# Performance work log

Measured on AMD Instinct MI355X. Metric: run time of the kernel, lower is better.

The kernel has to match this reference:

```python
import jax, jax.numpy as jnp
import numpy as np

# ---- constants (match init_kwargs) ----
H = 16            # bit depth of location codes
TP = 8            # number of parallel location dims
N = 1 << H        # location magnitude bound
N_K = 2
N_C = 2 * H * N_K + 1   # 65 candidate locations per token
T = 512           # T_train
N_TTNBR = 64
K_VOCAB = 128
S = N_TTNBR + K_VOCAB   # 192
D = 256           # dim_eu
TEMP = 0.05


def cos_similarity(c1, c2):
    """CritiGraph frexp-based cosine: sign product * (1 - bitlength(|a|^|b| + 1)/h)."""
    sg = (2 * (c1 >= 0).astype(jnp.int32) - 1) * (2 * (c2 >= 0).astype(jnp.int32) - 1)
    x = jnp.abs(c1) ^ jnp.abs(c2)
    _, e = jnp.frexp((x + 1).astype(jnp.float32))  # exponent == bit_length(x+1)
    return sg.astype(jnp.float32) * (1.0 - e.astype(jnp.float32) / H)


def setup_inputs() -> dict:
    key = jax.random.key(0)
    ks = jax.random.split(key, 8)
    loc = lambda k, shape: jax.random.randint(k, shape, 1 - N, N, dtype=jnp.int32)
    return {
        "cur_tar": jax.random.randint(ks[0], (T,), 0, K_VOCAB, dtype=jnp.int32),
        "cnc_loc": loc(ks[1], (T, N_C, TP)),
        "sta_loc": loc(ks[2], (T, TP)),
        "ttn_loc": loc(ks[3], (T, N_TTNBR, TP)),
        "voc_loc": loc(ks[4], (T, K_VOCAB, TP)),
        "sta_emb": 0.1 * jax.random.normal(ks[5], (T, D), dtype=jnp.float32),
        "ttn_emb": 0.1 * jax.random.normal(ks[6], (T, N_TTNBR, D), dtype=jnp.float32),
        "voc_emb": 0.1 * jax.random.normal(ks[7], (T, K_VOCAB, D), dtype=jnp.float32),
    }


def reference(cur_tar, cnc_loc, sta_loc, ttn_loc, voc_loc, sta_emb, ttn_emb, voc_emb):
    # positives = dynamic neighbors ++ sampled vocab
    pos_loc = jnp.concatenate([ttn_loc, voc_loc], axis=1)      # (T, S, TP) int32
    pos_emb = jnp.concatenate([ttn_emb, voc_emb], axis=1)      # (T, S, D)

    # Euclidean-space logits
    eu_val = 20.0 * TEMP * jnp.einsum('td,tsd->ts', sta_emb, pos_emb)  # (T, S)

    # CT-space similarities
    cos_sp = cos_similarity(sta_loc[:, None, :], pos_loc)      # (T, S, TP)
    cos_sum = cos_sp.sum(axis=-1)                              # (T, S)
    # candidate location swapped into each track d (ct_val_triton math)
    cos_cp = cos_similarity(cnc_loc[:, None, :, :], pos_loc[:, :, None, :])  # (T, S, N_C, TP)
    ct_val = (cos_sum[:, :, None, None] - cos_sp[:, :, None, :] + cos_cp) / TP \
             * (20.0 * TEMP)                                   # (T, S, N_C, TP)

    # KL(eu || ct) over the dynamic neighbors
    logits_ct_dyn = ct_val[:, :N_TTNBR]                        # (T, Nn, N_C, TP)
    logits_eu_dyn = eu_val[:, :N_TTNBR]                        # (T, Nn)
    p_eu = jax.nn.softmax(logits_eu_dyn, axis=1)
    lp_eu = jax.nn.log_softmax(logits_eu_dyn, axis=1)
    lp_ct = jax.nn.log_softmax(logits_ct_dyn, axis=1)
    loss_dyn_dyn = (p_eu[:, :, None, None] * (lp_eu[:, :, None, None] - lp_ct)).sum(axis=1)  # (T, N_C, TP)

    # cross-entropy over the sampled vocab
    logits_ct_sta = ct_val[:, N_TTNBR:] / TEMP                 # (T, K, N_C, TP)
    logits_flat = logits_ct_sta.reshape(T, K_VOCAB, N_C * TP)
    log_probs = jax.nn.log_softmax(logits_flat, axis=1)        # (T, K, N_C*TP)
    idx = jnp.broadcast_to(cur_tar[:, None, None].astype(jnp.int32), (T, 1, N_C * TP))
    target_lp = jnp.take_along_axis(log_probs, idx, axis=1)[:, 0, :]  # (T, N_C*TP)
    loss_dyn_sta = -target_lp.reshape(T, N_C, TP)              # (T, N_C, TP)

    return loss_dyn_dyn, loss_dyn_sta
```

## Files before the change

### kernel.cpp

```cpp
#include <hip/hip_runtime.h>


#define Tn   512
#define NC   65
#define TPd  8
#define NTn  64
#define KV   128
#define Sn   192
#define Dn   256
#define OUT1 (Tn * NC * TPd)
#define TABN 34
#define TABR (TABN * 32)

#define LOG2E 1.44269504088896340736f
#define LN2   0.69314718055994530942f
#define K1S (0.0625f * 2.5f * LOG2E)
#define K0S (-2.5f * LOG2E)

__device__ __forceinline__ float exp2_fast(float x) {
#if __has_builtin(__builtin_amdgcn_exp2f)
    return __builtin_amdgcn_exp2f(x);
#else
    return exp2f(x);
#endif
}
__device__ __forceinline__ int pack_loc(int v) {
    return (v < 0) ? (int)(0x80000000u | (unsigned)(-v)) : v;
}
__device__ __forceinline__ float asf(int v) { return __int_as_float(v); }

__device__ __forceinline__ float cos_raw(int y) {
    int   x = (y & 0x7fffffff) + 1;
    float c = fmaf((float)__clz(x), 0.0625f, -1.0f);
    return __int_as_float(__float_as_int(c) ^ (y & 0x80000000));
}
__device__ __forceinline__ int tab_idx(int y) {
    int x = (y & 0x7fffffff) + 1;
    int u = __clz(x) - 15;
    return u * 2 + (int)(((unsigned)y) >> 31);
}

__global__ __launch_bounds__(512, 4) void critigraph_kernel(
    const int*   __restrict__ cur_tar,
    const int*   __restrict__ cnc_loc,
    const int*   __restrict__ sta_loc,
    const int*   __restrict__ ttn_loc,
    const int*   __restrict__ voc_loc,
    const float* __restrict__ sta_emb,
    const float* __restrict__ ttn_emb,
    float*       __restrict__ out)
{
    __shared__ int4  s_dyn4[NTn * TPd];
    __shared__ int2  s_sta2[KV * TPd];
    __shared__ float s_tab[3 * TABR];
    __shared__ int   s_cnc[NC * TPd];
    __shared__ int   s_staloc[TPd];
    __shared__ float s_csum[Sn];
    __shared__ float s_eu[NTn];
    __shared__ float s_peu[NTn];
    __shared__ float s_dotbase[TPd];
    __shared__ float s_kl;

    const int t   = blockIdx.x;
    const int tid = threadIdx.x;

    if (tid < TPd) s_staloc[tid] = pack_loc(sta_loc[t * TPd + tid]);
    for (int i = tid; i < NC * TPd; i += 512)
        s_cnc[i] = pack_loc(cnc_loc[t * NC * TPd + i]);
    for (int i = tid; i < TABR; i += 512) {
        int   idx = i >> 5;
        int   clz = 15 + (idx >> 1);
        float mag = (float)clz * 0.0625f - 1.0f;
        float sgn = (idx & 1) ? -1.f : 1.f;
        float ccd = sgn * mag * (0.125f * LOG2E);
        float ccs = sgn * mag * (2.5f * LOG2E);
        s_tab[i]            = exp2_fast(ccd);
        s_tab[i + TABR]     = ccd;
        s_tab[i + 2 * TABR] = exp2_fast(ccs);
    }
    __syncthreads();

    const int mysta = s_staloc[tid & 7];
    float mysp[3];
    #pragma unroll
    for (int k = 0; k < 3; ++k) {
        int i = tid + 512 * k;
        int s = i >> 3;
        int v = (s < NTn) ? ttn_loc[t * NTn * TPd + i]
                          : voc_loc[t * KV * TPd + (i - NTn * TPd)];
        int packed = pack_loc(v);
        float c = cos_raw(packed ^ mysta);
        mysp[k] = c;
        if (s < NTn) s_dyn4[i].x = packed;
        else         s_sta2[i - NTn * TPd].x = packed;
        float v8 = c;
        v8 += __shfl_xor(v8, 1);
        v8 += __shfl_xor(v8, 2);
        v8 += __shfl_xor(v8, 4);
        if ((tid & 7) == 0) s_csum[s] = v8;
    }
    {
        const int r = tid >> 3, q = tid & 7;
        const float4* A = (const float4*)(sta_emb + (size_t)t * Dn);
        const float4* B = (const float4*)(ttn_emb + ((size_t)t * NTn + r) * Dn);
        float acc = 0.f;
        #pragma unroll
        for (int k = 0; k < 8; ++k) {
            float4 a = A[k * 8 + q];
            float4 b = B[k * 8 + q];
            acc += a.x * b.x + a.y * b.y + a.z * b.z + a.w * b.w;
        }
        acc += __shfl_xor(acc, 1);
        acc += __shfl_xor(acc, 2);
        acc += __shfl_xor(acc, 4);
        if (q == 0) s_eu[r] = acc;
    }
    __syncthreads();

    #pragma unroll
    for (int k = 0; k < 3; ++k) {
        int i = tid + 512 * k;
        int s = i >> 3;
        if (s < NTn) {
            float b2 = (s_csum[s] - mysp[k]) * (0.125f * LOG2E);
            s_dyn4[i].y = __float_as_int(exp2_fast(b2));
            s_dyn4[i].w = __float_as_int(b2);
        } else {
            float b2 = (s_csum[s] - mysp[k]) * (2.5f * LOG2E);
            s_sta2[i - NTn * TPd].y = __float_as_int(exp2_fast(b2));
        }
    }
    if (tid < 64) {
        float e  = s_eu[tid];
        float mx = e;
        #pragma unroll
        for (int m = 1; m < 64; m <<= 1) mx = fmaxf(mx, __shfl_xor(mx, m));
        float ex = __expf(e - mx);
        float z  = ex;
        #pragma unroll
        for (int m = 1; m < 64; m <<= 1) z += __shfl_xor(z, m);
        float pe = ex / z;
        s_peu[tid] = pe;
        float kls = pe * ((e - mx) - __logf(z));
        #pragma unroll
        for (int m = 1; m < 64; m <<= 1) kls += __shfl_xor(kls, m);
        if (tid == 0) s_kl = kls;
    }
    __syncthreads();

    s_dyn4[tid].z = __float_as_int(s_peu[tid >> 3]);
    if (tid < 64) {
        int g = tid & 7, j = tid >> 3;
        float a = 0.f;
        #pragma unroll
        for (int k = 0; k < 8; ++k) {
            int s = 8 * j + k;
            a = fmaf(s_peu[s], asf(s_dyn4[s * TPd + g].w), a);
        }
        #pragma unroll
        for (int m = 8; m < 64; m <<= 1) a += __shfl_xor(a, m);
        if (tid < TPd) s_dotbase[g] = a;
    }
    __syncthreads();

    const int   p    = tid & 7;
    const int   acnc = s_cnc[tid];
    const int   tar  = cur_tar[t];
    const float kl   = s_kl;
    const float dtb  = s_dotbase[p];
    const float* tb  = s_tab + (tid & 31);

    float sum = 0.f, dot = 0.f;
    #pragma unroll 16
    for (int s = 0; s < NTn; ++s) {
        int4  ab  = s_dyn4[s * TPd + p];
        int   j   = tab_idx(ab.x ^ acnc) * 32;
        float eD  = tb[j];
        float ccD = tb[j + TABR];
        sum = fmaf(asf(ab.y), eD, sum);
        dot = fmaf(asf(ab.z), ccD, dot);
    }
    float s2 = 0.f;
    #pragma unroll 16
    for (int v = 0; v < KV; ++v) {
        int2  ab = s_sta2[v * TPd + p];
        int   j  = tab_idx(ab.x ^ acnc) * 32;
        s2 = fmaf(asf(ab.y), tb[j + 2 * TABR], s2);
    }
    {
        int   ax  = s_sta2[tar * TPd + p].x;
        float sp  = cos_raw(ax ^ s_staloc[p]);
        float b2t = (s_csum[NTn + tar] - sp) * (2.5f * LOG2E);
        int   y   = ax ^ acnc;
        int   x   = (y & 0x7fffffff) + 1;
        float cct = fmaf((float)__clz(x), K1S, K0S);
        cct = __int_as_float(__float_as_int(cct) ^ (y & 0x80000000));
        float* od = out + (size_t)t * NC * TPd;
        float* os = out + OUT1 + (size_t)t * NC * TPd;
        od[tid] = kl + LN2 * (__log2f(sum) - (dtb + dot));
        os[tid] = LN2 * (__log2f(s2) - (b2t + cct));
    }

    {
        const int w    = tid >> 6;
        const int lane = tid & 63;
        const int acw  = s_cnc[512 + w];
        float sumd, dotd, sums;
        {
            int4  ab = s_dyn4[lane * TPd + w];
            int   j  = tab_idx(ab.x ^ acw) * 32;
            sumd = asf(ab.y) * tb[j];
            dotd = asf(ab.z) * tb[j + TABR];
        }
        {
            int2 ab0 = s_sta2[lane * TPd + w];
            int2 ab1 = s_sta2[(lane + 64) * TPd + w];
            int  j0  = tab_idx(ab0.x ^ acw) * 32;
            int  j1  = tab_idx(ab1.x ^ acw) * 32;
            sums = asf(ab0.y) * tb[j0 + 2 * TABR] + asf(ab1.y) * tb[j1 + 2 * TABR];
        }
        #pragma unroll
        for (int m = 1; m < 64; m <<= 1) {
            sumd += __shfl_xor(sumd, m);
            dotd += __shfl_xor(dotd, m);
            sums += __shfl_xor(sums, m);
        }
        if (lane == 0) {
            int   ax  = s_sta2[tar * TPd + w].x;
            float sp  = cos_raw(ax ^ s_staloc[w]);
            float b2t = (s_csum[NTn + tar] - sp) * (2.5f * LOG2E);
            int   y   = ax ^ acw;
            int   x   = (y & 0x7fffffff) + 1;
            float cct = fmaf((float)__clz(x), K1S, K0S);
            cct = __int_as_float(__float_as_int(cct) ^ (y & 0x80000000));
            out[(size_t)t * NC * TPd + 512 + w] =
                kl + LN2 * (__log2f(sumd) - (s_dotbase[w] + dotd));
            out[OUT1 + (size_t)t * NC * TPd + 512 + w] =
                LN2 * (__log2f(sums) - (b2t + cct));
        }
    }
}

extern "C" void kernel_launch(void* const* d_in, const int* in_sizes, int n_in,
                              void* d_out, int out_size, void* d_ws, size_t ws_size,
                              hipStream_t stream) {
    (void)in_sizes; (void)n_in; (void)d_ws; (void)ws_size; (void)out_size;
    const int*   cur_tar = (const int*)  d_in[0];
    const int*   cnc_loc = (const int*)  d_in[1];
    const int*   sta_loc = (const int*)  d_in[2];
    const int*   ttn_loc = (const int*)  d_in[3];
    const int*   voc_loc = (const int*)  d_in[4];
    const float* sta_emb = (const float*)d_in[5];
    const float* ttn_emb = (const float*)d_in[6];
    critigraph_kernel<<<Tn, 512, 0, stream>>>(cur_tar, cnc_loc, sta_loc, ttn_loc,
                                              voc_loc, sta_emb, ttn_emb, (float*)d_out);
}
```

Measured before the change: 143.5 us.

## Replace LDS exp lookup tables with inline clz math and packed bf16 operands

Drops the per-block shared-memory lookup tables and computes the cosine term and its exp2 inline from clz on a new shifted sign-magnitude packing. Shared data is laid out so two positives sit in one int4, and the dynamic-neighbour exp and softmax weights are packed as two rounded 16-bit halves in one word. This halves LDS traffic in the main loops and removes the table-building pass, at the cost of more ALU and transcendental work per element. The bf16 rounding of the exp and probability factors lowers precision, which may break accuracy tolerances.

```diff
diff --git a/kernel.cpp b/kernel.cpp
--- a/kernel.cpp
+++ b/kernel.cpp
@@ -9,13 +9,12 @@
 #define Sn   192
 #define Dn   256
 #define OUT1 (Tn * NC * TPd)
-#define TABN 34
-#define TABR (TABN * 32)
 
 #define LOG2E 1.44269504088896340736f
 #define LN2   0.69314718055994530942f
-#define K1S (0.0625f * 2.5f * LOG2E)
-#define K0S (-2.5f * LOG2E)
+#define ADYN (0.125f * LOG2E * 0.0625f)
+#define ASTA (2.5f  * LOG2E * 0.0625f)
+#define ARAW 0.0625f
 
 __device__ __forceinline__ float exp2_fast(float x) {
 #if __has_builtin(__builtin_amdgcn_exp2f)
@@ -24,20 +23,21 @@
     return exp2f(x);
 #endif
 }
-__device__ __forceinline__ int pack_loc(int v) {
-    return (v < 0) ? (int)(0x80000000u | (unsigned)(-v)) : v;
-}
 __device__ __forceinline__ float asf(int v) { return __int_as_float(v); }
-
-__device__ __forceinline__ float cos_raw(int y) {
-    int   x = (y & 0x7fffffff) + 1;
-    float c = fmaf((float)__clz(x), 0.0625f, -1.0f);
-    return __int_as_float(__float_as_int(c) ^ (y & 0x80000000));
-}
-__device__ __forceinline__ int tab_idx(int y) {
-    int x = (y & 0x7fffffff) + 1;
-    int u = __clz(x) - 15;
-    return u * 2 + (int)(((unsigned)y) >> 31);
+__device__ __forceinline__ int   asi(float v) { return __float_as_int(v); }
+
+__device__ __forceinline__ int pack15(int v) {
+    int a = (v < 0) ? -v : v;
+    return (a << 15) | (int)(((unsigned)v) >> 31);
+}
+__device__ __forceinline__ float cos15(int y, float A) {
+    int   x = y + 0x8000;
+    float c = fmaf((float)__clz(x), A, -A);
+    return asf(asi(c) ^ (y << 31));
+}
+
+__device__ __forceinline__ int eidx(int s, int p) {
+    return ((s >> 1) * TPd + p) * 2 + (s & 1);
 }
 
 __global__ __launch_bounds__(512, 4) void critigraph_kernel(
@@ -50,9 +50,9 @@
     const float* __restrict__ ttn_emb,
     float*       __restrict__ out)
 {
-    __shared__ int4  s_dyn4[NTn * TPd];
+    __shared__ int2  s_dyn2[NTn * TPd];
     __shared__ int2  s_sta2[KV * TPd];
-    __shared__ float s_tab[3 * TABR];
+    __shared__ float s_b2d[NTn * TPd];
     __shared__ int   s_cnc[NC * TPd];
     __shared__ int   s_staloc[TPd];
     __shared__ float s_csum[Sn];
@@ -63,21 +63,11 @@
 
     const int t   = blockIdx.x;
     const int tid = threadIdx.x;
-
-    if (tid < TPd) s_staloc[tid] = pack_loc(sta_loc[t * TPd + tid]);
+    const int tar = cur_tar[t];
+
+    if (tid < TPd) s_staloc[tid] = pack15(sta_loc[t * TPd + tid]);
     for (int i = tid; i < NC * TPd; i += 512)
-        s_cnc[i] = pack_loc(cnc_loc[t * NC * TPd + i]);
-    for (int i = tid; i < TABR; i += 512) {
-        int   idx = i >> 5;
-        int   clz = 15 + (idx >> 1);
-        float mag = (float)clz * 0.0625f - 1.0f;
-        float sgn = (idx & 1) ? -1.f : 1.f;
-        float ccd = sgn * mag * (0.125f * LOG2E);
-        float ccs = sgn * mag * (2.5f * LOG2E);
-        s_tab[i]            = exp2_fast(ccd);
-        s_tab[i + TABR]     = ccd;
-        s_tab[i + 2 * TABR] = exp2_fast(ccs);
-    }
+        s_cnc[i] = pack15(cnc_loc[t * NC * TPd + i]);
     __syncthreads();
 
     const int mysta = s_staloc[tid & 7];
@@ -86,18 +76,19 @@
     for (int k = 0; k < 3; ++k) {
         int i = tid + 512 * k;
         int s = i >> 3;
+        int p = i & 7;
         int v = (s < NTn) ? ttn_loc[t * NTn * TPd + i]
                           : voc_loc[t * KV * TPd + (i - NTn * TPd)];
-        int packed = pack_loc(v);
-        float c = cos_raw(packed ^ mysta);
+        int packed = pack15(v);
+        float c = cos15(packed ^ mysta, ARAW);
         mysp[k] = c;
-        if (s < NTn) s_dyn4[i].x = packed;
-        else         s_sta2[i - NTn * TPd].x = packed;
+        if (s < NTn) s_dyn2[eidx(s, p)].x = packed;
+        else         s_sta2[eidx(s - NTn, p)].x = packed;
         float v8 = c;
         v8 += __shfl_xor(v8, 1);
         v8 += __shfl_xor(v8, 2);
         v8 += __shfl_xor(v8, 4);
-        if ((tid & 7) == 0) s_csum[s] = v8;
+        if (p == 0) s_csum[s] = v8;
     }
     {
         const int r = tid >> 3, q = tid & 7;
@@ -121,13 +112,15 @@
     for (int k = 0; k < 3; ++k) {
         int i = tid + 512 * k;
         int s = i >> 3;
+        int p = i & 7;
         if (s < NTn) {
             float b2 = (s_csum[s] - mysp[k]) * (0.125f * LOG2E);
-            s_dyn4[i].y = __float_as_int(exp2_fast(b2));
-            s_dyn4[i].w = __float_as_int(b2);
+            int   e  = eidx(s, p);
+            s_dyn2[e].y = asi(exp2_fast(b2));
+            s_b2d[e]    = b2;
         } else {
             float b2 = (s_csum[s] - mysp[k]) * (2.5f * LOG2E);
-            s_sta2[i - NTn * TPd].y = __float_as_int(exp2_fast(b2));
+            s_sta2[eidx(s - NTn, p)].y = asi(exp2_fast(b2));
         }
     }
     if (tid < 64) {
@@ -148,14 +141,21 @@
     }
     __syncthreads();
 
-    s_dyn4[tid].z = __float_as_int(s_peu[tid >> 3]);
+    {
+        int i = tid;
+        int s = (((i >> 4) << 1) | (i & 1));
+        int Eb = s_dyn2[i].y;
+        int Pb = asi(s_peu[s]);
+        s_dyn2[i].y = (int)((((unsigned)Eb + 0x8000u) & 0xFFFF0000u) |
+                            (((unsigned)Pb + 0x8000u) >> 16));
+    }
     if (tid < 64) {
         int g = tid & 7, j = tid >> 3;
         float a = 0.f;
         #pragma unroll
         for (int k = 0; k < 8; ++k) {
             int s = 8 * j + k;
-            a = fmaf(s_peu[s], asf(s_dyn4[s * TPd + g].w), a);
+            a = fmaf(s_peu[s], s_b2d[eidx(s, g)], a);
         }
         #pragma unroll
         for (int m = 8; m < 64; m <<= 1) a += __shfl_xor(a, m);
@@ -165,36 +165,43 @@
 
     const int   p    = tid & 7;
     const int   acnc = s_cnc[tid];
-    const int   tar  = cur_tar[t];
     const float kl   = s_kl;
     const float dtb  = s_dotbase[p];
-    const float* tb  = s_tab + (tid & 31);
+    const int4* dyn4 = (const int4*)s_dyn2;
+    const int4* sta4 = (const int4*)s_sta2;
 
     float sum = 0.f, dot = 0.f;
-    #pragma unroll 16
-    for (int s = 0; s < NTn; ++s) {
-        int4  ab  = s_dyn4[s * TPd + p];
-        int   j   = tab_idx(ab.x ^ acnc) * 32;
-        float eD  = tb[j];
-        float ccD = tb[j + TABR];
-        sum = fmaf(asf(ab.y), eD, sum);
-        dot = fmaf(asf(ab.z), ccD, dot);
+    #pragma unroll 8
+    for (int j = 0; j < NTn / 2; ++j) {
+        int4 q = dyn4[j * TPd + p];
+        {
+            int   y  = q.x ^ acnc;
+            float cc = cos15(y, ADYN);
+            float E  = asf(q.y & (int)0xFFFF0000);
+            float pe = asf(q.y << 16);
+            sum = fmaf(E, exp2_fast(cc), sum);
+            dot = fmaf(pe, cc, dot);
+        }
+        {
+            int   y  = q.z ^ acnc;
+            float cc = cos15(y, ADYN);
+            float E  = asf(q.w & (int)0xFFFF0000);
+            float pe = asf(q.w << 16);
+            sum = fmaf(E, exp2_fast(cc), sum);
+            dot = fmaf(pe, cc, dot);
+        }
     }
     float s2 = 0.f;
-    #pragma unroll 16
-    for (int v = 0; v < KV; ++v) {
-        int2  ab = s_sta2[v * TPd + p];
-        int   j  = tab_idx(ab.x ^ acnc) * 32;
-        s2 = fmaf(asf(ab.y), tb[j + 2 * TABR], s2);
-    }
-    {
-        int   ax  = s_sta2[tar * TPd + p].x;
-        float sp  = cos_raw(ax ^ s_staloc[p]);
-        float b2t = (s_csum[NTn + tar] - sp) * (2.5f * LOG2E);
-        int   y   = ax ^ acnc;
-        int   x   = (y & 0x7fffffff) + 1;
-        float cct = fmaf((float)__clz(x), K1S, K0S);
-        cct = __int_as_float(__float_as_int(cct) ^ (y & 0x80000000));
+    #pragma unroll 8
+    for (int j = 0; j < KV / 2; ++j) {
+        int4 q = sta4[j * TPd + p];
+        s2 = fmaf(asf(q.y), exp2_fast(cos15(q.x ^ acnc, ASTA)), s2);
+        s2 = fmaf(asf(q.w), exp2_fast(cos15(q.z ^ acnc, ASTA)), s2);
+    }
+    {
+        int2  tq  = s_sta2[eidx(tar, p)];
+        float b2t = __log2f(asf(tq.y));
+        float cct = cos15(tq.x ^ acnc, ASTA);
         float* od = out + (size_t)t * NC * TPd;
         float* os = out + OUT1 + (size_t)t * NC * TPd;
         od[tid] = kl + LN2 * (__log2f(sum) - (dtb + dot));
@@ -207,17 +214,17 @@
         const int acw  = s_cnc[512 + w];
         float sumd, dotd, sums;
         {
-            int4  ab = s_dyn4[lane * TPd + w];
-            int   j  = tab_idx(ab.x ^ acw) * 32;
-            sumd = asf(ab.y) * tb[j];
-            dotd = asf(ab.z) * tb[j + TABR];
-        }
-        {
-            int2 ab0 = s_sta2[lane * TPd + w];
-            int2 ab1 = s_sta2[(lane + 64) * TPd + w];
-            int  j0  = tab_idx(ab0.x ^ acw) * 32;
-            int  j1  = tab_idx(ab1.x ^ acw) * 32;
-            sums = asf(ab0.y) * tb[j0 + 2 * TABR] + asf(ab1.y) * tb[j1 + 2 * TABR];
+            int2  q  = s_dyn2[eidx(lane, w)];
+            int   y  = q.x ^ acw;
+            float cc = cos15(y, ADYN);
+            sumd = asf(q.y & (int)0xFFFF0000) * exp2_fast(cc);
+            dotd = asf(q.y << 16) * cc;
+        }
+        {
+            int2 q0 = s_sta2[eidx(lane, w)];
+            int2 q1 = s_sta2[eidx(lane + 64, w)];
+            sums = asf(q0.y) * exp2_fast(cos15(q0.x ^ acw, ASTA))
+                 + asf(q1.y) * exp2_fast(cos15(q1.x ^ acw, ASTA));
         }
         #pragma unroll
         for (int m = 1; m < 64; m <<= 1) {
@@ -226,13 +233,9 @@
             sums += __shfl_xor(sums, m);
         }
         if (lane == 0) {
-            int   ax  = s_sta2[tar * TPd + w].x;
-            float sp  = cos_raw(ax ^ s_staloc[w]);
-            float b2t = (s_csum[NTn + tar] - sp) * (2.5f * LOG2E);
-            int   y   = ax ^ acw;
-            int   x   = (y & 0x7fffffff) + 1;
-            float cct = fmaf((float)__clz(x), K1S, K0S);
-            cct = __int_as_float(__float_as_int(cct) ^ (y & 0x80000000));
+            int2  tq  = s_sta2[eidx(tar, w)];
+            float b2t = __log2f(asf(tq.y));
+            float cct = cos15(tq.x ^ acw, ASTA);
             out[(size_t)t * NC * TPd + 512 + w] =
                 kl + LN2 * (__log2f(sumd) - (s_dotbase[w] + dotd));
             out[OUT1 + (size_t)t * NC * TPd + 512 + w] =
```

After: 143.0 us. No clear change (-0.3%).
